# Optimization experiments

Measured on AMD Instinct MI355X. Metric: run time of the kernel, lower is better.

## Reference

```python
import jax, jax.numpy as jnp
import numpy as np

B, S, D, H = 2, 2048, 1024, 16
HW = D // H  # head width = 64


def setup_inputs() -> dict:
    key = jax.random.key(0)
    ks = jax.random.split(key, 9)
    x = jax.random.normal(ks[0], (B, S, D), dtype=jnp.float32)
    mask = jax.random.randint(ks[1], (B, S), 0, 2, dtype=jnp.int32)
    pos = jax.random.normal(ks[2], (B, S, S), dtype=jnp.float32) * 0.02
    wq = jax.random.normal(ks[3], (D, D), dtype=jnp.float32) * 0.02
    bq = jnp.zeros((D,), dtype=jnp.float32)
    wk = jax.random.normal(ks[4], (D, D), dtype=jnp.float32) * 0.02
    bk = jnp.zeros((D,), dtype=jnp.float32)
    wv = jax.random.normal(ks[5], (D, D), dtype=jnp.float32) * 0.02
    bv = jnp.zeros((D,), dtype=jnp.float32)
    return {"x": x, "mask": mask, "pos": pos,
            "wq": wq, "bq": bq, "wk": wk, "bk": bk, "wv": wv, "bv": bv}


def reference(x, mask, pos, wq, bq, wk, bk, wv, bv):
    # QKV projections (torch Linear: y = x @ W^T + b)
    q = (x @ wq.T + bq).reshape(B, S, H, HW)
    k = (x @ wk.T + bk).reshape(B, S, H, HW)
    v = (x @ wv.T + bv).reshape(B, S, H, HW)
    # scores: (B, H, Sq, Sk)
    scores = jnp.einsum('bqhd,bkhd->bhqk', q, k) / jnp.sqrt(jnp.float32(HW))
    scores = scores + pos[:, None, :, :]
    m = mask.astype(jnp.float32)[:, None, None, :]
    scores = scores - 10000.0 * (1.0 - m)
    attn = jax.nn.softmax(scores, axis=-1)  # dropout p=0 (inference)
    h = jnp.einsum('bhqk,bkhd->bqhd', attn, v).reshape(B, S, D)
    return h
```

## Files before the change

### kernel.cpp

```cpp
#include <hip/hip_runtime.h>

#define B_ 2
#define S_ 2048
#define D_ 1024
#define H_ 16
#define HW_ 64
#define NT_ (S_ / 64)

typedef __attribute__((ext_vector_type(8))) short s16x8;
typedef __attribute__((ext_vector_type(4))) float f32x4;
typedef __attribute__((ext_vector_type(4))) unsigned int u32x4;

__device__ __forceinline__ unsigned short f2bf(float f) {
  unsigned int x = __builtin_bit_cast(unsigned int, f);
  x += 0x7fffu + ((x >> 16) & 1u);
  return (unsigned short)(x >> 16);
}
__device__ __forceinline__ float bf2f(unsigned short u) {
  unsigned int x = ((unsigned int)u) << 16;
  return __builtin_bit_cast(float, x);
}
__device__ __forceinline__ unsigned int cvtpk_bf16(float lo, float hi) {
  unsigned int r;
  asm("v_cvt_pk_bf16_f32 %0, %1, %2" : "=v"(r) : "v"(lo), "v"(hi));
  return r;
}
__device__ __forceinline__ void gload16(const void* g, void* l) {
  __builtin_amdgcn_global_load_lds(
      (const __attribute__((address_space(1))) unsigned int*)g,
      (__attribute__((address_space(3))) unsigned int*)l, 16, 0, 0);
}

__global__ __launch_bounds__(256) void cvt_all(const float* __restrict__ x,
                                               const float* __restrict__ wq,
                                               const float* __restrict__ wk,
                                               const float* __restrict__ wv,
                                               const float* __restrict__ pos,
                                               const int* __restrict__ mask,
                                               unsigned short* __restrict__ xb,
                                               unsigned short* __restrict__ wb,
                                               unsigned short* __restrict__ posb) {
  const int blk = blockIdx.x;
  if (blk < 2048) {
    int i = blk * 256 + threadIdx.x;
    const float4* s = (const float4*)x;
    float4 a = s[2 * i], b = s[2 * i + 1];
    s16x8 o;
    o[0] = (short)f2bf(a.x); o[1] = (short)f2bf(a.y);
    o[2] = (short)f2bf(a.z); o[3] = (short)f2bf(a.w);
    o[4] = (short)f2bf(b.x); o[5] = (short)f2bf(b.y);
    o[6] = (short)f2bf(b.z); o[7] = (short)f2bf(b.w);
    ((s16x8*)xb)[i] = o;
  } else if (blk < 3584) {
    int blk2 = blk - 2048;
    const float* src = (blk2 < 512) ? wq : (blk2 < 1024) ? wk : wv;
    int i = (blk2 & 511) * 256 + threadIdx.x;
    const float4* s = (const float4*)src;
    float4 a = s[2 * i], b = s[2 * i + 1];
    s16x8 o;
    o[0] = (short)f2bf(a.x); o[1] = (short)f2bf(a.y);
    o[2] = (short)f2bf(a.z); o[3] = (short)f2bf(a.w);
    o[4] = (short)f2bf(b.x); o[5] = (short)f2bf(b.y);
    o[6] = (short)f2bf(b.z); o[7] = (short)f2bf(b.w);
    ((s16x8*)wb)[(size_t)(blk2 >> 9) * (D_ * D_ / 8) + i] = o;
  } else {
    int i = (blk - 3584) * 256 + threadIdx.x;
    int e = i * 8;
    int b = e / (S_ * S_);
    int k = e & (S_ - 1);
    const float4* s = (const float4*)pos;
    float4 a = s[2 * i], c = s[2 * i + 1];
    const int* mrow = mask + b * S_ + k;
    const float L2E = 1.4426950408889634f;
    float f[8] = {a.x, a.y, a.z, a.w, c.x, c.y, c.z, c.w};
    s16x8 o;
#pragma unroll
    for (int j = 0; j < 8; ++j) {
      float bias = mrow[j] ? 0.0f : -14427.0f;
      o[j] = (short)f2bf(f[j] * L2E + bias);
    }
    ((s16x8*)posb)[i] = o;
  }
}

__global__ __launch_bounds__(256) void qkv_gemm(const unsigned short* __restrict__ X,
                                                const unsigned short* __restrict__ W3,
                                                const float* __restrict__ bq,
                                                const float* __restrict__ bk,
                                                const float* __restrict__ bv,
                                                unsigned short* __restrict__ O3,
                                                unsigned short* __restrict__ VT) {
  const int mat = blockIdx.z;
  const unsigned short* Wp = W3 + (size_t)mat * (D_ * D_);
  const float* bias = (mat == 0) ? bq : (mat == 1) ? bk : bv;
  unsigned short* Op = O3 + (size_t)mat * ((size_t)B_ * S_ * D_);

  const int bm = blockIdx.y * 128, bn = blockIdx.x * 128;
  const int tid = threadIdx.x;
  const int lane = tid & 63, w = tid >> 6;
  const int wr = (w >> 1) * 64, wc = (w & 1) * 64;
  const int l15 = lane & 15, lh = lane >> 4;

  __shared__ __align__(16) unsigned short Al[128 * 64];
  __shared__ __align__(16) unsigned short Wl[128 * 64];

  f32x4 acc[4][4];
#pragma unroll
  for (int m = 0; m < 4; ++m)
#pragma unroll
    for (int n = 0; n < 4; ++n) acc[m][n] = (f32x4){0.f, 0.f, 0.f, 0.f};

  const int srow = lane >> 3;
  const int scol = ((lane & 7) ^ srow) * 8;
  const int i0 = w * 4;

  for (int k0 = 0; k0 < D_; k0 += 64) {
    __syncthreads();
#pragma unroll
    for (int i2 = 0; i2 < 4; ++i2) {
      int i = i0 + i2;
      int row = 8 * i + srow;
      gload16(X + (size_t)(bm + row) * D_ + k0 + scol, Al + i * 512);
      gload16(Wp + (size_t)(bn + row) * D_ + k0 + scol, Wl + i * 512);
    }
    __syncthreads();
#pragma unroll
    for (int kb = 0; kb < 2; ++kb) {
      const int cs = (kb * 32 + lh * 8) ^ ((l15 & 7) * 8);
      s16x8 af[4], wf[4];
#pragma unroll
      for (int m = 0; m < 4; ++m)
        af[m] = *(const s16x8*)(Al + (wr + m * 16 + l15) * 64 + cs);
#pragma unroll
      for (int n = 0; n < 4; ++n)
        wf[n] = *(const s16x8*)(Wl + (wc + n * 16 + l15) * 64 + cs);
      if (mat == 2) {
#pragma unroll
        for (int m = 0; m < 4; ++m)
#pragma unroll
          for (int n = 0; n < 4; ++n)
            acc[m][n] =
                __builtin_amdgcn_mfma_f32_16x16x32_bf16(wf[n], af[m], acc[m][n], 0, 0, 0);
      } else {
#pragma unroll
        for (int m = 0; m < 4; ++m)
#pragma unroll
          for (int n = 0; n < 4; ++n)
            acc[m][n] =
                __builtin_amdgcn_mfma_f32_16x16x32_bf16(af[m], wf[n], acc[m][n], 0, 0, 0);
      }
    }
  }

  if (mat == 2) {
#pragma unroll
    for (int n = 0; n < 4; ++n) {
      f32x4 b4 = *(const f32x4*)(bias + bn + wc + n * 16 + lh * 4);
#pragma unroll
      for (int m = 0; m < 4; ++m) {
        int t = bm + wr + m * 16 + l15;
        int bb = t >> 11, s = t & (S_ - 1);
#pragma unroll
        for (int r = 0; r < 4; ++r) {
          int f = bn + wc + n * 16 + lh * 4 + r;
          VT[((size_t)(bb * H_ + (f >> 6)) * HW_ + (f & 63)) * S_ + s] =
              f2bf(acc[m][n][r] + b4[r]);
        }
      }
    }
  } else {
    const float oscale = (mat == 0) ? 0.18033688751411092f : 1.0f;
#pragma unroll
    for (int n = 0; n < 4; ++n) {
      int col = bn + wc + n * 16 + l15;
      float bval = bias[col];
#pragma unroll
      for (int m = 0; m < 4; ++m) {
        int row0 = bm + wr + m * 16 + lh * 4;
#pragma unroll
        for (int r = 0; r < 4; ++r)
          Op[(size_t)(row0 + r) * D_ + col] = f2bf((acc[m][n][r] + bval) * oscale);
      }
    }
  }
}

__global__ __launch_bounds__(256, 4) void attn_kernel(
    const unsigned short* __restrict__ Q,
    const unsigned short* __restrict__ K,
    const unsigned short* __restrict__ VT,
    const unsigned short* __restrict__ POSM,
    float* __restrict__ OUT) {
  const int h = blockIdx.x, qt = blockIdx.y, b = blockIdx.z;
  const int tid = threadIdx.x;
  const int lane = tid & 63, w = tid >> 6;
  const int l15 = lane & 15, lh = lane >> 4;
  const int qp = w >> 1, kh = w & 1;

  __shared__ __align__(16) unsigned short Kl[2][64 * 64];
  __shared__ __align__(16) unsigned short Vl[2][64 * 64];

  const int swzk = ((l15 & 3) | (((l15 >> 2) & 1) << 2)) * 8;
  const int swzv = ((l15 & 3) | ((l15 & 8) >> 1)) * 8;
  const int rowbase = kh * 32 + 8 * (l15 >> 2) + (l15 & 3);

  const int srow = lane >> 3;
  const int scol = ((lane & 7) ^ ((lane >> 3) & 3) ^ ((w & 1) << 2)) * 8;
  const unsigned short* Kbase = K + (size_t)b * S_ * D_ + h * HW_;
  const unsigned short* Vbase = VT + ((size_t)(b * H_ + h) * HW_) * S_;

  auto stage = [&](int buf, int kt) {
    const int k0 = kt * 64;
#pragma unroll
    for (int i = 0; i < 2; ++i) {
      const int rb = i * 32 + w * 8;
      gload16(Kbase + (size_t)(k0 + rb + srow) * D_ + scol, &Kl[buf][rb * 64]);
      gload16(Vbase + (size_t)(rb + srow) * S_ + k0 + scol, &Vl[buf][rb * 64]);
    }
  };

  const int q0 = qt * 64 + qp * 32;
  const int qg0 = q0 + l15, qg1 = q0 + 16 + l15;
  const unsigned short* Pp0 = POSM + (size_t)(b * S_ + qg0) * S_ + kh * 32 + lh * 8;
  const unsigned short* Pp1 = POSM + (size_t)(b * S_ + qg1) * S_ + kh * 32 + lh * 8;

  stage(0, 0);
  s16x8 pm_c[2], pm_n[2];
  pm_c[0] = *(const s16x8*)(Pp0);
  pm_c[1] = *(const s16x8*)(Pp1);

  s16x8 qf[2][2];
  {
    const unsigned short* qp0 = Q + (size_t)(b * S_ + qg0) * D_ + h * HW_ + lh * 8;
    const unsigned short* qp1 = Q + (size_t)(b * S_ + qg1) * D_ + h * HW_ + lh * 8;
    qf[0][0] = *(const s16x8*)qp0;
    qf[0][1] = *(const s16x8*)(qp0 + 32);
    qf[1][0] = *(const s16x8*)qp1;
    qf[1][1] = *(const s16x8*)(qp1 + 32);
  }

  f32x4 Oc[2][4];
#pragma unroll
  for (int s = 0; s < 2; ++s)
#pragma unroll
    for (int n = 0; n < 4; ++n) Oc[s][n] = (f32x4){0.f, 0.f, 0.f, 0.f};
  float lsq[2] = {0.f, 0.f};

  for (int kt = 0; kt < NT_; ++kt) {
    const int cur = kt & 1;

    asm volatile("s_waitcnt vmcnt(2)" ::: "memory");
    asm volatile("s_barrier" ::: "memory");

    if (kt + 1 < NT_) {
      stage(cur ^ 1, kt + 1);
      pm_n[0] = *(const s16x8*)(Pp0 + (kt + 1) * 64);
      pm_n[1] = *(const s16x8*)(Pp1 + (kt + 1) * 64);
    }

    const unsigned short* Kc = Kl[cur];
    const unsigned short* Vc = Vl[cur];

    s16x8 kf0[2], kf1[2];
#pragma unroll
    for (int n = 0; n < 2; ++n) {
      const unsigned short* kr = Kc + (rowbase + n * 4) * 64;
      kf0[n] = *(const s16x8*)(kr + ((lh * 8) ^ swzk));
      kf1[n] = *(const s16x8*)(kr + ((32 + lh * 8) ^ swzk));
    }

    f32x4 sc[2][2];
    __builtin_amdgcn_s_setprio(1);
#pragma unroll
    for (int s = 0; s < 2; ++s)
#pragma unroll
      for (int n = 0; n < 2; ++n) {
        f32x4 c;
#pragma unroll
        for (int r = 0; r < 4; ++r)
          c[r] = bf2f((unsigned short)pm_c[s][n * 4 + r]);
        c = __builtin_amdgcn_mfma_f32_16x16x32_bf16(kf0[n], qf[s][0], c, 0, 0, 0);
        c = __builtin_amdgcn_mfma_f32_16x16x32_bf16(kf1[n], qf[s][1], c, 0, 0, 0);
        sc[s][n] = c;
      }
    __builtin_amdgcn_s_setprio(0);

    s16x8 vf[4];
#pragma unroll
    for (int n = 0; n < 4; ++n)
      vf[n] = *(const s16x8*)(Vc + (n * 16 + l15) * 64 + ((kh * 32 + lh * 8) ^ swzv));

#pragma unroll
    for (int s = 0; s < 2; ++s)
#pragma unroll
      for (int n = 0; n < 2; ++n)
#pragma unroll
        for (int r = 0; r < 4; ++r) {
          float p = __builtin_amdgcn_exp2f(sc[s][n][r]);
          sc[s][n][r] = p;
          lsq[s] += p;
        }

    __builtin_amdgcn_s_setprio(1);
#pragma unroll
    for (int s = 0; s < 2; ++s) {
      u32x4 pw;
      pw[0] = cvtpk_bf16(sc[s][0][0], sc[s][0][1]);
      pw[1] = cvtpk_bf16(sc[s][0][2], sc[s][0][3]);
      pw[2] = cvtpk_bf16(sc[s][1][0], sc[s][1][1]);
      pw[3] = cvtpk_bf16(sc[s][1][2], sc[s][1][3]);
      s16x8 pf = __builtin_bit_cast(s16x8, pw);
#pragma unroll
      for (int n = 0; n < 4; ++n)
        Oc[s][n] = __builtin_amdgcn_mfma_f32_16x16x32_bf16(vf[n], pf, Oc[s][n], 0, 0, 0);
    }
    __builtin_amdgcn_s_setprio(0);

    pm_c[0] = pm_n[0];
    pm_c[1] = pm_n[1];
  }

#pragma unroll
  for (int s = 0; s < 2; ++s) {
    lsq[s] += __shfl_xor(lsq[s], 16, 64);
    lsq[s] += __shfl_xor(lsq[s], 32, 64);
  }

  __syncthreads();
  f32x4* xO = (f32x4*)Kl;
  float* xL = (float*)Vl;
  if (kh) {
#pragma unroll
    for (int s = 0; s < 2; ++s) {
#pragma unroll
      for (int n = 0; n < 4; ++n)
        xO[((qp * 2 + s) * 4 + n) * 64 + lane] = Oc[s][n];
      if (lh == 0) xL[(qp * 2 + s) * 16 + l15] = lsq[s];
    }
  }
  __syncthreads();
  if (!kh) {
#pragma unroll
    for (int s = 0; s < 2; ++s) {
      float ltot = lsq[s] + xL[(qp * 2 + s) * 16 + l15];
      float inv = 1.0f / ltot;
      int qg = q0 + s * 16 + l15;
      float* outp = OUT + (size_t)(b * S_ + qg) * D_ + h * HW_ + lh * 4;
#pragma unroll
      for (int n = 0; n < 4; ++n) {
        f32x4 o = xO[((qp * 2 + s) * 4 + n) * 64 + lane];
#pragma unroll
        for (int r = 0; r < 4; ++r) o[r] = (o[r] + Oc[s][n][r]) * inv;
        *(f32x4*)(outp + n * 16) = o;
      }
    }
  }
}

extern "C" void kernel_launch(void* const* d_in, const int* in_sizes, int n_in,
                              void* d_out, int out_size, void* d_ws, size_t ws_size,
                              hipStream_t stream) {
  const float* x   = (const float*)d_in[0];
  const int*   msk = (const int*)d_in[1];
  const float* pos = (const float*)d_in[2];
  const float* wq  = (const float*)d_in[3];
  const float* bq  = (const float*)d_in[4];
  const float* wk  = (const float*)d_in[5];
  const float* bk  = (const float*)d_in[6];
  const float* wv  = (const float*)d_in[7];
  const float* bv  = (const float*)d_in[8];
  float* out = (float*)d_out;

  char* ws = (char*)d_ws;
  unsigned short* xb   = (unsigned short*)(ws);
  unsigned short* wb   = (unsigned short*)(ws + 8388608);
  unsigned short* qkv  = (unsigned short*)(ws + 14680064);
  unsigned short* posb = (unsigned short*)(ws + 31457280);
  unsigned short* vt   = (unsigned short*)(ws + 48234496);

  cvt_all<<<7680, 256, 0, stream>>>(x, wq, wk, wv, pos, msk, xb, wb, posb);

  qkv_gemm<<<dim3(D_ / 128, (B_ * S_) / 128, 3), 256, 0, stream>>>(
      xb, wb, bq, bk, bv, qkv, vt);

  attn_kernel<<<dim3(H_, S_ / 64, B_), 256, 0, stream>>>(
      qkv, qkv + (size_t)B_ * S_ * D_, vt, posb, out);
}
```

Before: 118.9 us.

## Software-pipeline attention loop so PV of previous tile overlaps QK of current

Restructures the attention main loop into a prologue, a steady state and an epilogue. Each iteration now issues the QK^T MFMAs for tile kt alongside the PV MFMAs for tile kt-1, so exp2 and bf16 packing overlap matrix work. V gets a third LDS buffer because its consumption lags K by one tile. The pos-bias loads move from register double-buffering to an in-iteration load followed by a full vmcnt(0) wait, which may expose more global-load latency and uses more LDS and registers.

```diff
diff --git a/kernel.cpp b/kernel.cpp
--- a/kernel.cpp
+++ b/kernel.cpp
@@ -15,10 +15,6 @@
   unsigned int x = __builtin_bit_cast(unsigned int, f);
   x += 0x7fffu + ((x >> 16) & 1u);
   return (unsigned short)(x >> 16);
-}
-__device__ __forceinline__ float bf2f(unsigned short u) {
-  unsigned int x = ((unsigned int)u) << 16;
-  return __builtin_bit_cast(float, x);
 }
 __device__ __forceinline__ unsigned int cvtpk_bf16(float lo, float hi) {
   unsigned int r;
@@ -198,7 +194,7 @@
   const int qp = w >> 1, kh = w & 1;
 
   __shared__ __align__(16) unsigned short Kl[2][64 * 64];
-  __shared__ __align__(16) unsigned short Vl[2][64 * 64];
+  __shared__ __align__(16) unsigned short Vl[3][64 * 64];
 
   const int swzk = ((l15 & 3) | (((l15 >> 2) & 1) << 2)) * 8;
   const int swzv = ((l15 & 3) | ((l15 & 8) >> 1)) * 8;
@@ -209,12 +205,19 @@
   const unsigned short* Kbase = K + (size_t)b * S_ * D_ + h * HW_;
   const unsigned short* Vbase = VT + ((size_t)(b * H_ + h) * HW_) * S_;
 
-  auto stage = [&](int buf, int kt) {
+  auto Kst = [&](int buf, int kt) {
     const int k0 = kt * 64;
 #pragma unroll
     for (int i = 0; i < 2; ++i) {
       const int rb = i * 32 + w * 8;
       gload16(Kbase + (size_t)(k0 + rb + srow) * D_ + scol, &Kl[buf][rb * 64]);
+    }
+  };
+  auto Vst = [&](int buf, int kt) {
+    const int k0 = kt * 64;
+#pragma unroll
+    for (int i = 0; i < 2; ++i) {
+      const int rb = i * 32 + w * 8;
       gload16(Vbase + (size_t)(rb + srow) * S_ + k0 + scol, &Vl[buf][rb * 64]);
     }
   };
@@ -224,10 +227,8 @@
   const unsigned short* Pp0 = POSM + (size_t)(b * S_ + qg0) * S_ + kh * 32 + lh * 8;
   const unsigned short* Pp1 = POSM + (size_t)(b * S_ + qg1) * S_ + kh * 32 + lh * 8;
 
-  stage(0, 0);
-  s16x8 pm_c[2], pm_n[2];
-  pm_c[0] = *(const s16x8*)(Pp0);
-  pm_c[1] = *(const s16x8*)(Pp1);
+  Kst(0, 0);
+  Vst(0, 0);
 
   s16x8 qf[2][2];
   {
@@ -246,21 +247,16 @@
     for (int n = 0; n < 4; ++n) Oc[s][n] = (f32x4){0.f, 0.f, 0.f, 0.f};
   float lsq[2] = {0.f, 0.f};
 
-  for (int kt = 0; kt < NT_; ++kt) {
-    const int cur = kt & 1;
-
-    asm volatile("s_waitcnt vmcnt(2)" ::: "memory");
+  u32x4 pfa, pfb;
+
+  {
+    asm volatile("s_waitcnt vmcnt(0)" ::: "memory");
     asm volatile("s_barrier" ::: "memory");
-
-    if (kt + 1 < NT_) {
-      stage(cur ^ 1, kt + 1);
-      pm_n[0] = *(const s16x8*)(Pp0 + (kt + 1) * 64);
-      pm_n[1] = *(const s16x8*)(Pp1 + (kt + 1) * 64);
-    }
-
-    const unsigned short* Kc = Kl[cur];
-    const unsigned short* Vc = Vl[cur];
-
+    u32x4 pm0 = *(const u32x4*)(Pp0);
+    u32x4 pm1 = *(const u32x4*)(Pp1);
+    Kst(1, 1);
+    Vst(1, 1);
+    const unsigned short* Kc = Kl[0];
     s16x8 kf0[2], kf1[2];
 #pragma unroll
     for (int n = 0; n < 2; ++n) {
@@ -268,28 +264,23 @@
       kf0[n] = *(const s16x8*)(kr + ((lh * 8) ^ swzk));
       kf1[n] = *(const s16x8*)(kr + ((32 + lh * 8) ^ swzk));
     }
-
     f32x4 sc[2][2];
     __builtin_amdgcn_s_setprio(1);
 #pragma unroll
-    for (int s = 0; s < 2; ++s)
+    for (int s = 0; s < 2; ++s) {
+      const u32x4 pmv = s ? pm1 : pm0;
 #pragma unroll
       for (int n = 0; n < 2; ++n) {
         f32x4 c;
-#pragma unroll
-        for (int r = 0; r < 4; ++r)
-          c[r] = bf2f((unsigned short)pm_c[s][n * 4 + r]);
+        c[0] = __builtin_bit_cast(float, pmv[n * 2] << 16);
+        c[1] = __builtin_bit_cast(float, pmv[n * 2] & 0xffff0000u);
+        c[2] = __builtin_bit_cast(float, pmv[n * 2 + 1] << 16);
+        c[3] = __builtin_bit_cast(float, pmv[n * 2 + 1] & 0xffff0000u);
         c = __builtin_amdgcn_mfma_f32_16x16x32_bf16(kf0[n], qf[s][0], c, 0, 0, 0);
-        c = __builtin_amdgcn_mfma_f32_16x16x32_bf16(kf1[n], qf[s][1], c, 0, 0, 0);
-        sc[s][n] = c;
-      }
+        sc[s][n] = __builtin_amdgcn_mfma_f32_16x16x32_bf16(kf1[n], qf[s][1], c, 0, 0, 0);
+      }
+    }
     __builtin_amdgcn_s_setprio(0);
-
-    s16x8 vf[4];
-#pragma unroll
-    for (int n = 0; n < 4; ++n)
-      vf[n] = *(const s16x8*)(Vc + (n * 16 + l15) * 64 + ((kh * 32 + lh * 8) ^ swzv));
-
 #pragma unroll
     for (int s = 0; s < 2; ++s)
 #pragma unroll
@@ -300,24 +291,104 @@
           sc[s][n][r] = p;
           lsq[s] += p;
         }
-
+    pfa[0] = cvtpk_bf16(sc[0][0][0], sc[0][0][1]);
+    pfa[1] = cvtpk_bf16(sc[0][0][2], sc[0][0][3]);
+    pfa[2] = cvtpk_bf16(sc[0][1][0], sc[0][1][1]);
+    pfa[3] = cvtpk_bf16(sc[0][1][2], sc[0][1][3]);
+    pfb[0] = cvtpk_bf16(sc[1][0][0], sc[1][0][1]);
+    pfb[1] = cvtpk_bf16(sc[1][0][2], sc[1][0][3]);
+    pfb[2] = cvtpk_bf16(sc[1][1][0], sc[1][1][1]);
+    pfb[3] = cvtpk_bf16(sc[1][1][2], sc[1][1][3]);
+  }
+
+  for (int kt = 1; kt < NT_; ++kt) {
+    asm volatile("s_waitcnt vmcnt(0)" ::: "memory");
+    asm volatile("s_barrier" ::: "memory");
+
+    u32x4 pm0 = *(const u32x4*)(Pp0 + kt * 64);
+    u32x4 pm1 = *(const u32x4*)(Pp1 + kt * 64);
+    if (kt + 1 < NT_) {
+      Kst((kt + 1) & 1, kt + 1);
+      Vst((kt + 1) % 3, kt + 1);
+    }
+
+    const unsigned short* Kc = Kl[kt & 1];
+    const unsigned short* Vp = Vl[(kt - 1) % 3];
+    s16x8 kf0[2], kf1[2];
+#pragma unroll
+    for (int n = 0; n < 2; ++n) {
+      const unsigned short* kr = Kc + (rowbase + n * 4) * 64;
+      kf0[n] = *(const s16x8*)(kr + ((lh * 8) ^ swzk));
+      kf1[n] = *(const s16x8*)(kr + ((32 + lh * 8) ^ swzk));
+    }
+    s16x8 vf[4];
+#pragma unroll
+    for (int n = 0; n < 4; ++n)
+      vf[n] = *(const s16x8*)(Vp + (n * 16 + l15) * 64 + ((kh * 32 + lh * 8) ^ swzv));
+
+    f32x4 sc[2][2];
     __builtin_amdgcn_s_setprio(1);
 #pragma unroll
     for (int s = 0; s < 2; ++s) {
-      u32x4 pw;
-      pw[0] = cvtpk_bf16(sc[s][0][0], sc[s][0][1]);
-      pw[1] = cvtpk_bf16(sc[s][0][2], sc[s][0][3]);
-      pw[2] = cvtpk_bf16(sc[s][1][0], sc[s][1][1]);
-      pw[3] = cvtpk_bf16(sc[s][1][2], sc[s][1][3]);
-      s16x8 pf = __builtin_bit_cast(s16x8, pw);
+      const u32x4 pmv = s ? pm1 : pm0;
+#pragma unroll
+      for (int n = 0; n < 2; ++n) {
+        f32x4 c;
+        c[0] = __builtin_bit_cast(float, pmv[n * 2] << 16);
+        c[1] = __builtin_bit_cast(float, pmv[n * 2] & 0xffff0000u);
+        c[2] = __builtin_bit_cast(float, pmv[n * 2 + 1] << 16);
+        c[3] = __builtin_bit_cast(float, pmv[n * 2 + 1] & 0xffff0000u);
+        c = __builtin_amdgcn_mfma_f32_16x16x32_bf16(kf0[n], qf[s][0], c, 0, 0, 0);
+        sc[s][n] = __builtin_amdgcn_mfma_f32_16x16x32_bf16(kf1[n], qf[s][1], c, 0, 0, 0);
+      }
+    }
+
+    {
+      s16x8 pfa8 = __builtin_bit_cast(s16x8, pfa);
+      s16x8 pfb8 = __builtin_bit_cast(s16x8, pfb);
 #pragma unroll
       for (int n = 0; n < 4; ++n)
-        Oc[s][n] = __builtin_amdgcn_mfma_f32_16x16x32_bf16(vf[n], pf, Oc[s][n], 0, 0, 0);
+        Oc[0][n] = __builtin_amdgcn_mfma_f32_16x16x32_bf16(vf[n], pfa8, Oc[0][n], 0, 0, 0);
+#pragma unroll
+      for (int n = 0; n < 4; ++n)
+        Oc[1][n] = __builtin_amdgcn_mfma_f32_16x16x32_bf16(vf[n], pfb8, Oc[1][n], 0, 0, 0);
     }
     __builtin_amdgcn_s_setprio(0);
 
-    pm_c[0] = pm_n[0];
-    pm_c[1] = pm_n[1];
+#pragma unroll
+    for (int s = 0; s < 2; ++s)
+#pragma unroll
+      for (int n = 0; n < 2; ++n)
+#pragma unroll
+        for (int r = 0; r < 4; ++r) {
+          float p = __builtin_amdgcn_exp2f(sc[s][n][r]);
+          sc[s][n][r] = p;
+          lsq[s] += p;
+        }
+    pfa[0] = cvtpk_bf16(sc[0][0][0], sc[0][0][1]);
+    pfa[1] = cvtpk_bf16(sc[0][0][2], sc[0][0][3]);
+    pfa[2] = cvtpk_bf16(sc[0][1][0], sc[0][1][1]);
+    pfa[3] = cvtpk_bf16(sc[0][1][2], sc[0][1][3]);
+    pfb[0] = cvtpk_bf16(sc[1][0][0], sc[1][0][1]);
+    pfb[1] = cvtpk_bf16(sc[1][0][2], sc[1][0][3]);
+    pfb[2] = cvtpk_bf16(sc[1][1][0], sc[1][1][1]);
+    pfb[3] = cvtpk_bf16(sc[1][1][2], sc[1][1][3]);
+  }
+
+  {
+    const unsigned short* Vp = Vl[(NT_ - 1) % 3];
+    s16x8 vf[4];
+#pragma unroll
+    for (int n = 0; n < 4; ++n)
+      vf[n] = *(const s16x8*)(Vp + (n * 16 + l15) * 64 + ((kh * 32 + lh * 8) ^ swzv));
+    s16x8 pfa8 = __builtin_bit_cast(s16x8, pfa);
+    s16x8 pfb8 = __builtin_bit_cast(s16x8, pfb);
+#pragma unroll
+    for (int n = 0; n < 4; ++n)
+      Oc[0][n] = __builtin_amdgcn_mfma_f32_16x16x32_bf16(vf[n], pfa8, Oc[0][n], 0, 0, 0);
+#pragma unroll
+    for (int n = 0; n < 4; ++n)
+      Oc[1][n] = __builtin_amdgcn_mfma_f32_16x16x32_bf16(vf[n], pfb8, Oc[1][n], 0, 0, 0);
   }
 
 #pragma unroll
```

New measurement: 120.7 us. Within noise of the previous version (+1.5%).
